# Performance work log

Measured on AMD Instinct MI355X. Metric: run time of the kernel, lower is better.

## Reference

```python
import jax, jax.numpy as jnp
import numpy as np

EMBED_DIM = 1024
NUM_HEADS = 16
HEAD_DIM = EMBED_DIM // NUM_HEADS
SCALE = HEAD_DIM ** 0.5


def setup_inputs() -> dict:
    key = jax.random.key(0)
    kx, kq, kk, kv, ko = jax.random.split(key, 5)
    B, S, D = 4, 2048, EMBED_DIM
    std = 1.0 / np.sqrt(D)
    return {
        "x": jax.random.normal(kx, (B, S, D), dtype=jnp.float32),
        "W_q": jax.random.normal(kq, (D, D), dtype=jnp.float32) * std,
        "W_k": jax.random.normal(kk, (D, D), dtype=jnp.float32) * std,
        "W_v": jax.random.normal(kv, (D, D), dtype=jnp.float32) * std,
        "W_o": jax.random.normal(ko, (D, D), dtype=jnp.float32) * std,
    }


def reference(x, W_q, W_k, W_v, W_o):
    B, S, D = x.shape
    H, Hd = NUM_HEADS, HEAD_DIM

    def split(t):  # [B,S,D] -> [B,H,S,Hd]
        return t.reshape(B, S, H, Hd).transpose(0, 2, 1, 3)

    # nn.Linear stores weight as [out,in] and computes x @ W.T
    Q = split(x @ W_q.T)
    K = split(x @ W_k.T)
    V = split(x @ W_v.T)

    scores = jnp.einsum("bhqd,bhkd->bhqk", Q, K) / SCALE
    causal = jnp.tril(jnp.ones((S, S), dtype=bool))
    scores = jnp.where(causal, scores, -jnp.inf)
    weights = jax.nn.softmax(scores, axis=-1)  # dropout p=0 (eval)
    out = jnp.einsum("bhqk,bhkd->bhqd", weights, V)
    out = out.transpose(0, 2, 1, 3).reshape(B, S, D)
    return out @ W_o.T
```

## Files before the change

### kernel.cpp

```cpp
#include <hip/hip_runtime.h>
#include <stdint.h>

#define DEV __device__ __forceinline__

typedef __bf16 bf16x8 __attribute__((ext_vector_type(8)));
typedef float f32x4 __attribute__((ext_vector_type(4)));

DEV ushort f2bf(float f) {
    union { float f; uint32_t u; } v; v.f = f;
    uint32_t r = v.u + 0x7FFFu + ((v.u >> 16) & 1u);
    return (ushort)(r >> 16);
}

DEV ushort bfc(float f) {
    union { __bf16 h; ushort u; } v;
    v.h = (__bf16)f;
    return v.u;
}

DEV void gld16(const void* g, void* lds) {
    __builtin_amdgcn_global_load_lds(
        (const __attribute__((address_space(1))) void*)g,
        (__attribute__((address_space(3))) void*)lds, 16, 0, 0);
}

DEV bf16x8 ld_frag(const void* p) { return *(const bf16x8*)p; }

__global__ void cvt_kernel(const float* __restrict__ in, ushort* __restrict__ out, int n4) {
    int i = blockIdx.x * blockDim.x + threadIdx.x;
    if (i >= n4) return;
    float4 v = ((const float4*)in)[i];
    ushort4 o;
    o.x = f2bf(v.x); o.y = f2bf(v.y); o.z = f2bf(v.z); o.w = f2bf(v.w);
    ((ushort4*)out)[i] = o;
}

__global__ void cvt4_kernel(const float* __restrict__ w0, const float* __restrict__ w1,
                            const float* __restrict__ w2, const float* __restrict__ w3,
                            ushort* __restrict__ out, int n4) {
    int i = blockIdx.x * blockDim.x + threadIdx.x;
    if (i >= n4) return;
    const float* src = (blockIdx.y == 0) ? w0 : (blockIdx.y == 1) ? w1
                     : (blockIdx.y == 2) ? w2 : w3;
    float4 v = ((const float4*)src)[i];
    ushort4 o;
    o.x = f2bf(v.x); o.y = f2bf(v.y); o.z = f2bf(v.z); o.w = f2bf(v.w);
    ((ushort4*)(out + (size_t)blockIdx.y * n4 * 4))[i] = o;
}

DEV void stage_half(const ushort* Mp, int grow0, int k0, char* ldsbase, int t, int K) {
#pragma unroll
    for (int i = 0; i < 2; ++i) {
        int o = (i * 512 + t) * 16;
        int row = o >> 7;
        int cs = ((o >> 4) & 7) ^ (row & 7);
        gld16((const char*)Mp + ((size_t)(grow0 + row) * K + k0) * 2 + cs * 16, ldsbase + o);
    }
}

DEV void gphase(const char* Ab, const char* Bb, f32x4 acc[8][4],
                int wr, int wc, int rA, int cc, int mh, int nh) {
    bf16x8 af[4][2], bg[2][2];
#pragma unroll
    for (int i2 = 0; i2 < 4; ++i2)
#pragma unroll
        for (int kc = 0; kc < 2; ++kc) {
            int ra = wr * 128 + mh * 64 + i2 * 16 + rA;
            af[i2][kc] = ld_frag(Ab + ra * 128 + (((kc * 4 + cc) ^ (ra & 7)) * 16));
        }
#pragma unroll
    for (int j2 = 0; j2 < 2; ++j2)
#pragma unroll
        for (int kc = 0; kc < 2; ++kc) {
            int rb = wc * 64 + nh * 32 + j2 * 16 + rA;
            bg[j2][kc] = ld_frag(Bb + rb * 128 + (((kc * 4 + cc) ^ (rb & 7)) * 16));
        }
    __builtin_amdgcn_s_setprio(1);
#pragma unroll
    for (int kc = 0; kc < 2; ++kc)
#pragma unroll
        for (int i2 = 0; i2 < 4; ++i2)
#pragma unroll
            for (int j2 = 0; j2 < 2; ++j2)
                acc[mh * 4 + i2][nh * 2 + j2] = __builtin_amdgcn_mfma_f32_16x16x32_bf16(
                    af[i2][kc], bg[j2][kc], acc[mh * 4 + i2][nh * 2 + j2], 0, 0, 0);
    __builtin_amdgcn_s_setprio(0);
}

template<int F32OUT>
__global__ __launch_bounds__(512, 2) void gemm256(const ushort* __restrict__ A,
                                                  const ushort* __restrict__ B,
                                                  void* __restrict__ C,
                                                  int M, int N, int K) {
    __shared__ __align__(16) ushort S[2][2][16384];
    const int G = gridDim.x;
    const int bid = blockIdx.x;
    const int swz = (bid & 7) * (G >> 3) + (bid >> 3);
    const int nbn = N >> 8;
    const int bm = swz / nbn, bn = swz % nbn;
    const int t = threadIdx.x, l = t & 63, w = t >> 6;
    const int wr = w >> 2, wc = w & 3;
    const int rA = l & 15, cc = l >> 4;
    f32x4 acc[8][4] = {};
    const int NT = K >> 6;

    stage_half(A, bm * 256,       0, (char*)S[0][0],         t, K);
    stage_half(A, bm * 256 + 128, 0, (char*)S[0][0] + 16384, t, K);
    stage_half(B, bn * 256,       0, (char*)S[0][1],         t, K);
    stage_half(B, bn * 256 + 128, 0, (char*)S[0][1] + 16384, t, K);
    asm volatile("s_waitcnt vmcnt(0)" ::: "memory");
    __builtin_amdgcn_s_barrier();

    for (int kt = 0; kt < NT; ++kt) {
        const int buf = kt & 1;
        const char* Ab = (const char*)S[buf][0];
        const char* Bb = (const char*)S[buf][1];
        char* An = (char*)S[buf ^ 1][0];
        char* Bn = (char*)S[buf ^ 1][1];
        const int k1 = (kt + 1) << 6;
        const bool more = (kt + 1 < NT);
        if (more) stage_half(A, bm * 256,       k1, An,         t, K);
        gphase(Ab, Bb, acc, wr, wc, rA, cc, 0, 0);
        if (more) stage_half(A, bm * 256 + 128, k1, An + 16384, t, K);
        gphase(Ab, Bb, acc, wr, wc, rA, cc, 0, 1);
        if (more) stage_half(B, bn * 256,       k1, Bn,         t, K);
        gphase(Ab, Bb, acc, wr, wc, rA, cc, 1, 0);
        if (more) stage_half(B, bn * 256 + 128, k1, Bn + 16384, t, K);
        gphase(Ab, Bb, acc, wr, wc, rA, cc, 1, 1);
        asm volatile("s_waitcnt vmcnt(0)" ::: "memory");
        __builtin_amdgcn_s_barrier();
    }

#pragma unroll
    for (int i = 0; i < 8; ++i)
#pragma unroll
        for (int j = 0; j < 4; ++j)
#pragma unroll
            for (int r = 0; r < 4; ++r) {
                int row = bm * 256 + wr * 128 + i * 16 + cc * 4 + r;
                int col = bn * 256 + wc * 64 + j * 16 + rA;
                if (F32OUT) ((float*)C)[(size_t)row * N + col] = acc[i][j][r];
                else        ((ushort*)C)[(size_t)row * N + col] = f2bf(acc[i][j][r]);
            }
}

template<int F32OUT>
__global__ __launch_bounds__(256) void gemm_bt(const ushort* __restrict__ A,
                                               const ushort* __restrict__ B,
                                               void* __restrict__ C,
                                               int M, int N, int K) {
    __shared__ __align__(16) ushort As[128 * 64];
    __shared__ __align__(16) ushort Bs[128 * 64];
    const int G = gridDim.x;
    const int bid = blockIdx.x;
    const int swz = (bid & 7) * (G >> 3) + (bid >> 3);
    const int bm = swz & 63, bn = swz >> 6;
    const int t = threadIdx.x, l = t & 63, w = t >> 6;
    const int wm = w >> 1, wn = w & 1;
    const int rA = l & 15, cc = l >> 4;
    f32x4 acc[4][4] = {};

    for (int k0 = 0; k0 < K; k0 += 64) {
#pragma unroll
        for (int i = 0; i < 4; ++i) {
            int o = (w * 4 + i) * 1024 + l * 16;
            int row = o >> 7, ch = (o >> 4) & 7;
            int cs = ch ^ (row & 7);
            const char* ga = (const char*)A + (((size_t)(bm * 128 + row)) * K + k0) * 2 + cs * 16;
            gld16(ga, (char*)As + (w * 4 + i) * 1024);
            const char* gb = (const char*)B + (((size_t)(bn * 128 + row)) * K + k0) * 2 + cs * 16;
            gld16(gb, (char*)Bs + (w * 4 + i) * 1024);
        }
        __syncthreads();
        bf16x8 af[4][2], bfr[4][2];
#pragma unroll
        for (int i = 0; i < 4; ++i) {
#pragma unroll
            for (int kc = 0; kc < 2; ++kc) {
                int ra = wm * 64 + i * 16 + rA;
                int ca = (kc * 4 + cc) ^ (ra & 7);
                af[i][kc] = ld_frag((const char*)As + ra * 128 + ca * 16);
                int rb = wn * 64 + i * 16 + rA;
                int cb = (kc * 4 + cc) ^ (rb & 7);
                bfr[i][kc] = ld_frag((const char*)Bs + rb * 128 + cb * 16);
            }
        }
#pragma unroll
        for (int kc = 0; kc < 2; ++kc)
#pragma unroll
            for (int i = 0; i < 4; ++i)
#pragma unroll
                for (int j = 0; j < 4; ++j)
                    acc[i][j] = __builtin_amdgcn_mfma_f32_16x16x32_bf16(
                        af[i][kc], bfr[j][kc], acc[i][j], 0, 0, 0);
        __syncthreads();
    }
#pragma unroll
    for (int i = 0; i < 4; ++i)
#pragma unroll
        for (int j = 0; j < 4; ++j)
#pragma unroll
            for (int r = 0; r < 4; ++r) {
                int row = bm * 128 + wm * 64 + i * 16 + cc * 4 + r;
                int col = bn * 128 + wn * 64 + j * 16 + rA;
                if (F32OUT) ((float*)C)[(size_t)row * N + col] = acc[i][j][r];
                else        ((ushort*)C)[(size_t)row * N + col] = f2bf(acc[i][j][r]);
            }
}

__global__ __launch_bounds__(256) void vtrans_kernel(const ushort* __restrict__ qkv,
                                                     ushort* __restrict__ vt) {
    __shared__ ushort tile[64][68];
    const int st = blockIdx.x, bh = blockIdx.y;
    const int b = bh >> 4, h = bh & 15;
    const int t = threadIdx.x;
    const ushort* src = qkv + (size_t)(b * 2048 + st * 64) * 3072 + 2048 + h * 64;
#pragma unroll
    for (int i = 0; i < 2; ++i) {
        int idx = t + i * 256;
        int s = idx >> 3, d0 = (idx & 7) * 8;
        uint4 v = *(const uint4*)(src + (size_t)s * 3072 + d0);
        *(uint2*)&tile[s][d0]     = make_uint2(v.x, v.y);
        *(uint2*)&tile[s][d0 + 4] = make_uint2(v.z, v.w);
    }
    __syncthreads();
    ushort* dst = vt + (size_t)bh * 64 * 2048 + st * 64;
#pragma unroll
    for (int i = 0; i < 2; ++i) {
        int idx = t + i * 256;
        int d = idx >> 3, s0 = (idx & 7) * 8;
        ushort tmp[8];
#pragma unroll
        for (int j = 0; j < 8; ++j) tmp[j] = tile[s0 + j][d];
        *(uint4*)(dst + (size_t)d * 2048 + s0) = *(uint4*)tmp;
    }
}

DEV void stage_kv(const char* Kg0, const char* Vg0, int kv0,
                  char* KsB, char* VsB, int t) {
    int row = t >> 3;
    int cs = (t & 7) ^ (row & 7);
    gld16(Kg0 + (size_t)(kv0 + row) * 6144 + cs * 16, KsB + t * 16);
    gld16(Vg0 + (size_t)row * 4096 + (size_t)kv0 * 2 + cs * 16, VsB + t * 16);
}

DEV void attn_tile(const char* KsB, const char* VsB, char* PsW,
                   const bf16x8* qf, f32x4* oacc, float& lsum,
                   int rA, int cc, int qg, int kv0, bool diag) {
    f32x4 s[4] = {};
    __builtin_amdgcn_s_setprio(1);
#pragma unroll
    for (int kc = 0; kc < 2; ++kc)
#pragma unroll
        for (int c = 0; c < 4; ++c) {
            int rk = c * 16 + rA;
            int ck = (kc * 4 + cc) ^ (rk & 7);
            bf16x8 ak = ld_frag(KsB + rk * 128 + ck * 16);
            s[c] = __builtin_amdgcn_mfma_f32_16x16x32_bf16(ak, qf[kc], s[c], 0, 0, 0);
        }
    __builtin_amdgcn_s_setprio(0);
    const float SC = 0.18033688011116013f;
    const int swz = (rA & 7) << 4;
#pragma unroll
    for (int c = 0; c < 4; ++c) {
        float pv[4];
#pragma unroll
        for (int r = 0; r < 4; ++r) {
            float v = s[c][r] * SC;
            if (diag && (kv0 + c * 16 + cc * 4 + r > qg)) v = -1e30f;
            pv[r] = __builtin_amdgcn_exp2f(v);
            lsum += pv[r];
        }
        union { ushort us[4]; uint2 u2; } pk;
        pk.us[0] = bfc(pv[0]); pk.us[1] = bfc(pv[1]);
        pk.us[2] = bfc(pv[2]); pk.us[3] = bfc(pv[3]);
        *(uint2*)(PsW + rA * 128 + ((32 * c + 8 * cc) ^ swz)) = pk.u2;
    }
    bf16x8 ap[2];
    ap[0] = ld_frag(PsW + rA * 128 + ((16 * cc) ^ swz));
    ap[1] = ld_frag(PsW + rA * 128 + ((64 + 16 * cc) ^ swz));
    __builtin_amdgcn_s_setprio(1);
#pragma unroll
    for (int kc = 0; kc < 2; ++kc)
#pragma unroll
        for (int g = 0; g < 4; ++g) {
            int rv = g * 16 + rA;
            int cv = (kc * 4 + cc) ^ (rv & 7);
            bf16x8 av = ld_frag(VsB + rv * 128 + cv * 16);
            oacc[g] = __builtin_amdgcn_mfma_f32_16x16x32_bf16(av, ap[kc], oacc[g], 0, 0, 0);
        }
    __builtin_amdgcn_s_setprio(0);
}

__global__ __launch_bounds__(512, 4) void attn_kernel(const ushort* __restrict__ qkv,
                                                      const ushort* __restrict__ vt,
                                                      ushort* __restrict__ o_out) {
    const int i = blockIdx.x;
    const int xcd = i & 7, slot = i >> 3;
    const int p = slot >> 3;
    const int bh = ((slot & 7) << 3) | xcd;
    const int ftq = 15 - p;
    const int b = bh >> 4, h = bh & 15;
    const int t = threadIdx.x, l = t & 63, w = t >> 6;
    const int rA = l & 15, cc = l >> 4;
    const int wq16 = w * 16;

    __shared__ __align__(16) ushort Ks[2][64 * 64];
    __shared__ __align__(16) ushort Vs[2][64 * 64];
    __shared__ __align__(16) ushort Ps[8][16 * 64];

    const size_t xbase = (size_t)(b * 2048) * 3072 + (size_t)h * 64;
    const char* Kg0 = (const char*)(qkv + xbase + 1024);
    const char* Vg0 = (const char*)(vt + (size_t)bh * 64 * 2048);

    const int qgN = p * 128 + wq16 + rA;
    const int qgF = ftq * 128 + wq16 + rA;

    bf16x8 qfN[2], qfF[2];
    {
        const ushort* qpN = qkv + xbase + (size_t)qgN * 3072;
        const ushort* qpF = qkv + xbase + (size_t)qgF * 3072;
        qfN[0] = *(const bf16x8*)(qpN + cc * 8);
        qfN[1] = *(const bf16x8*)(qpN + 32 + cc * 8);
        qfF[0] = *(const bf16x8*)(qpF + cc * 8);
        qfF[1] = *(const bf16x8*)(qpF + 32 + cc * 8);
    }
    f32x4 oN[4] = {}, oF[4] = {};
    float lN = 0.f, lF = 0.f;

    const int nkv = 32 - 2 * p;
    stage_kv(Kg0, Vg0, 0, (char*)Ks[0], (char*)Vs[0], t);
    asm volatile("s_waitcnt vmcnt(0)" ::: "memory");
    __builtin_amdgcn_s_barrier();

    for (int kt = 0; kt < nkv; ++kt) {
        const int cur = kt & 1;
        if (kt + 1 < nkv)
            stage_kv(Kg0, Vg0, (kt + 1) * 64, (char*)Ks[cur ^ 1], (char*)Vs[cur ^ 1], t);
        const char* KsB = (const char*)Ks[cur];
        const char* VsB = (const char*)Vs[cur];
        attn_tile(KsB, VsB, (char*)Ps[w], qfF, oF, lF, rA, cc, qgF, kt * 64, kt >= nkv - 2);
        if (kt <= 2 * p + 1)
            attn_tile(KsB, VsB, (char*)Ps[w], qfN, oN, lN, rA, cc, qgN, kt * 64, kt >= 2 * p);
        asm volatile("s_waitcnt vmcnt(0)" ::: "memory");
        __builtin_amdgcn_s_barrier();
    }

    float lf = lF; lf += __shfl_xor(lf, 16); lf += __shfl_xor(lf, 32);
    float ln = lN; ln += __shfl_xor(ln, 16); ln += __shfl_xor(ln, 32);
    const float rf = 1.0f / lf, rn = 1.0f / ln;
    const size_t obF = (size_t)(b * 2048 + qgF) * 1024 + h * 64;
    const size_t obN = (size_t)(b * 2048 + qgN) * 1024 + h * 64;
#pragma unroll
    for (int g = 0; g < 4; ++g) {
        union { ushort us[4]; uint2 u2; } pf, pn;
#pragma unroll
        for (int r = 0; r < 4; ++r) {
            pf.us[r] = bfc(oF[g][r] * rf);
            pn.us[r] = bfc(oN[g][r] * rn);
        }
        *(uint2*)(o_out + obF + 16 * g + 4 * cc) = pf.u2;
        *(uint2*)(o_out + obN + 16 * g + 4 * cc) = pn.u2;
    }
}

extern "C" void kernel_launch(void* const* d_in, const int* in_sizes, int n_in,
                              void* d_out, int out_size, void* d_ws, size_t ws_size,
                              hipStream_t stream) {
    const float* x  = (const float*)d_in[0];
    const float* Wq = (const float*)d_in[1];
    const float* Wk = (const float*)d_in[2];
    const float* Wv = (const float*)d_in[3];
    const float* Wo = (const float*)d_in[4];
    float* out = (float*)d_out;

    const int M = 8192, D = 1024;
    char* ws = (char*)d_ws;
    ushort* xo_bf = (ushort*)ws;
    ushort* wqkv  = (ushort*)(ws + (size_t)M * D * 2);
    ushort* wo_bf = (ushort*)(ws + (size_t)M * D * 2 + (size_t)3 * D * D * 2);
    ushort* qkv   = (ushort*)(ws + (size_t)M * D * 2 + (size_t)4 * D * D * 2);
    ushort* vt    = (ushort*)d_out;

    cvt_kernel<<<dim3(M * D / 4 / 256), 256, 0, stream>>>(x, xo_bf, M * D / 4);
    cvt4_kernel<<<dim3(D * D / 4 / 256, 4), 256, 0, stream>>>(Wq, Wk, Wv, Wo, wqkv, D * D / 4);

    gemm256<0><<<dim3((M / 256) * (3072 / 256)), 512, 0, stream>>>(xo_bf, wqkv, qkv, M, 3072, D);

    vtrans_kernel<<<dim3(32, 64), 256, 0, stream>>>(qkv, vt);

    attn_kernel<<<dim3(512), 512, 0, stream>>>(qkv, vt, xo_bf);

    gemm_bt<1><<<dim3((M / 128) * (D / 128)), 256, 0, stream>>>(xo_bf, wo_bf, out, M, D, D);
}
```

Measured before the change: 244.7 us.

## Fold softmax scale into W_q, compute row sums via MFMA, double-buffer out-proj GEMM

The softmax scale (1/sqrt(d)·log2e) is folded into W_q during bf16 conversion, which removes a per-element multiply in the attention tile. The per-row softmax denominator is now accumulated by an MFMA against a vector of ones instead of scalar adds and cross-lane shuffles. It uses the same bf16-rounded probabilities as the PV product. The 128x128 GEMM gains LDS double-buffering with prefetch of the next K tile and priority hints around its MFMAs. The 256x256 GEMM issues all next-tile loads before compute instead of interleaving them.

```diff
diff --git a/kernel.cpp b/kernel.cpp
--- a/kernel.cpp
+++ b/kernel.cpp
@@ -42,9 +42,11 @@
     if (i >= n4) return;
     const float* src = (blockIdx.y == 0) ? w0 : (blockIdx.y == 1) ? w1
                      : (blockIdx.y == 2) ? w2 : w3;
+    const float scl = (blockIdx.y == 0) ? 0.18033688011116013f : 1.0f;
     float4 v = ((const float4*)src)[i];
     ushort4 o;
-    o.x = f2bf(v.x); o.y = f2bf(v.y); o.z = f2bf(v.z); o.w = f2bf(v.w);
+    o.x = f2bf(v.x * scl); o.y = f2bf(v.y * scl);
+    o.z = f2bf(v.z * scl); o.w = f2bf(v.w * scl);
     ((ushort4*)(out + (size_t)blockIdx.y * n4 * 4))[i] = o;
 }
 
@@ -118,14 +120,15 @@
         char* An = (char*)S[buf ^ 1][0];
         char* Bn = (char*)S[buf ^ 1][1];
         const int k1 = (kt + 1) << 6;
-        const bool more = (kt + 1 < NT);
-        if (more) stage_half(A, bm * 256,       k1, An,         t, K);
+        if (kt + 1 < NT) {
+            stage_half(A, bm * 256,       k1, An,         t, K);
+            stage_half(A, bm * 256 + 128, k1, An + 16384, t, K);
+            stage_half(B, bn * 256,       k1, Bn,         t, K);
+            stage_half(B, bn * 256 + 128, k1, Bn + 16384, t, K);
+        }
         gphase(Ab, Bb, acc, wr, wc, rA, cc, 0, 0);
-        if (more) stage_half(A, bm * 256 + 128, k1, An + 16384, t, K);
         gphase(Ab, Bb, acc, wr, wc, rA, cc, 0, 1);
-        if (more) stage_half(B, bn * 256,       k1, Bn,         t, K);
         gphase(Ab, Bb, acc, wr, wc, rA, cc, 1, 0);
-        if (more) stage_half(B, bn * 256 + 128, k1, Bn + 16384, t, K);
         gphase(Ab, Bb, acc, wr, wc, rA, cc, 1, 1);
         asm volatile("s_waitcnt vmcnt(0)" ::: "memory");
         __builtin_amdgcn_s_barrier();
@@ -149,8 +152,8 @@
                                                const ushort* __restrict__ B,
                                                void* __restrict__ C,
                                                int M, int N, int K) {
-    __shared__ __align__(16) ushort As[128 * 64];
-    __shared__ __align__(16) ushort Bs[128 * 64];
+    __shared__ __align__(16) ushort As[2][128 * 64];
+    __shared__ __align__(16) ushort Bs[2][128 * 64];
     const int G = gridDim.x;
     const int bid = blockIdx.x;
     const int swz = (bid & 7) * (G >> 3) + (bid >> 3);
@@ -159,32 +162,43 @@
     const int wm = w >> 1, wn = w & 1;
     const int rA = l & 15, cc = l >> 4;
     f32x4 acc[4][4] = {};
-
-    for (int k0 = 0; k0 < K; k0 += 64) {
-#pragma unroll
-        for (int i = 0; i < 4; ++i) {
-            int o = (w * 4 + i) * 1024 + l * 16;
-            int row = o >> 7, ch = (o >> 4) & 7;
-            int cs = ch ^ (row & 7);
-            const char* ga = (const char*)A + (((size_t)(bm * 128 + row)) * K + k0) * 2 + cs * 16;
-            gld16(ga, (char*)As + (w * 4 + i) * 1024);
-            const char* gb = (const char*)B + (((size_t)(bn * 128 + row)) * K + k0) * 2 + cs * 16;
-            gld16(gb, (char*)Bs + (w * 4 + i) * 1024);
-        }
-        __syncthreads();
+    const int NT = K >> 6;
+
+#define STAGE_AB(k0, sb)                                                              \
+    {                                                                                  \
+        _Pragma("unroll")                                                              \
+        for (int i = 0; i < 4; ++i) {                                                  \
+            int o = (w * 4 + i) * 1024 + l * 16;                                       \
+            int row = o >> 7;                                                          \
+            int cs = ((o >> 4) & 7) ^ (row & 7);                                       \
+            gld16((const char*)A + (((size_t)(bm * 128 + row)) * K + (k0)) * 2 + cs * 16, \
+                  (char*)As[sb] + o);                                                  \
+            gld16((const char*)B + (((size_t)(bn * 128 + row)) * K + (k0)) * 2 + cs * 16, \
+                  (char*)Bs[sb] + o);                                                  \
+        }                                                                              \
+    }
+
+    STAGE_AB(0, 0);
+    asm volatile("s_waitcnt vmcnt(0)" ::: "memory");
+    __builtin_amdgcn_s_barrier();
+
+    for (int kt = 0; kt < NT; ++kt) {
+        const int sb = kt & 1;
+        if (kt + 1 < NT) STAGE_AB((kt + 1) << 6, sb ^ 1);
+        const char* Ab = (const char*)As[sb];
+        const char* Bb = (const char*)Bs[sb];
         bf16x8 af[4][2], bfr[4][2];
 #pragma unroll
         for (int i = 0; i < 4; ++i) {
 #pragma unroll
             for (int kc = 0; kc < 2; ++kc) {
                 int ra = wm * 64 + i * 16 + rA;
-                int ca = (kc * 4 + cc) ^ (ra & 7);
-                af[i][kc] = ld_frag((const char*)As + ra * 128 + ca * 16);
+                af[i][kc] = ld_frag(Ab + ra * 128 + (((kc * 4 + cc) ^ (ra & 7)) * 16));
                 int rb = wn * 64 + i * 16 + rA;
-                int cb = (kc * 4 + cc) ^ (rb & 7);
-                bfr[i][kc] = ld_frag((const char*)Bs + rb * 128 + cb * 16);
+                bfr[i][kc] = ld_frag(Bb + rb * 128 + (((kc * 4 + cc) ^ (rb & 7)) * 16));
             }
         }
+        __builtin_amdgcn_s_setprio(1);
 #pragma unroll
         for (int kc = 0; kc < 2; ++kc)
 #pragma unroll
@@ -193,8 +207,11 @@
                 for (int j = 0; j < 4; ++j)
                     acc[i][j] = __builtin_amdgcn_mfma_f32_16x16x32_bf16(
                         af[i][kc], bfr[j][kc], acc[i][j], 0, 0, 0);
-        __syncthreads();
-    }
+        __builtin_amdgcn_s_setprio(0);
+        asm volatile("s_waitcnt vmcnt(0)" ::: "memory");
+        __builtin_amdgcn_s_barrier();
+    }
+#undef STAGE_AB
 #pragma unroll
     for (int i = 0; i < 4; ++i)
 #pragma unroll
@@ -245,7 +262,7 @@
 }
 
 DEV void attn_tile(const char* KsB, const char* VsB, char* PsW,
-                   const bf16x8* qf, f32x4* oacc, float& lsum,
+                   const bf16x8* qf, f32x4* oacc, f32x4& osum, const bf16x8 ones,
                    int rA, int cc, int qg, int kv0, bool diag) {
     f32x4 s[4] = {};
     __builtin_amdgcn_s_setprio(1);
@@ -259,17 +276,15 @@
             s[c] = __builtin_amdgcn_mfma_f32_16x16x32_bf16(ak, qf[kc], s[c], 0, 0, 0);
         }
     __builtin_amdgcn_s_setprio(0);
-    const float SC = 0.18033688011116013f;
     const int swz = (rA & 7) << 4;
 #pragma unroll
     for (int c = 0; c < 4; ++c) {
         float pv[4];
 #pragma unroll
         for (int r = 0; r < 4; ++r) {
-            float v = s[c][r] * SC;
+            float v = s[c][r];
             if (diag && (kv0 + c * 16 + cc * 4 + r > qg)) v = -1e30f;
             pv[r] = __builtin_amdgcn_exp2f(v);
-            lsum += pv[r];
         }
         union { ushort us[4]; uint2 u2; } pk;
         pk.us[0] = bfc(pv[0]); pk.us[1] = bfc(pv[1]);
@@ -280,6 +295,8 @@
     ap[0] = ld_frag(PsW + rA * 128 + ((16 * cc) ^ swz));
     ap[1] = ld_frag(PsW + rA * 128 + ((64 + 16 * cc) ^ swz));
     __builtin_amdgcn_s_setprio(1);
+    osum = __builtin_amdgcn_mfma_f32_16x16x32_bf16(ones, ap[0], osum, 0, 0, 0);
+    osum = __builtin_amdgcn_mfma_f32_16x16x32_bf16(ones, ap[1], osum, 0, 0, 0);
 #pragma unroll
     for (int kc = 0; kc < 2; ++kc)
 #pragma unroll
@@ -325,8 +342,12 @@
         qfF[0] = *(const bf16x8*)(qpF + cc * 8);
         qfF[1] = *(const bf16x8*)(qpF + 32 + cc * 8);
     }
+    bf16x8 ones;
+#pragma unroll
+    for (int z = 0; z < 8; ++z) ones[z] = (__bf16)1.0f;
+
     f32x4 oN[4] = {}, oF[4] = {};
-    float lN = 0.f, lF = 0.f;
+    f32x4 osN = {}, osF = {};
 
     const int nkv = 32 - 2 * p;
     stage_kv(Kg0, Vg0, 0, (char*)Ks[0], (char*)Vs[0], t);
@@ -339,16 +360,14 @@
             stage_kv(Kg0, Vg0, (kt + 1) * 64, (char*)Ks[cur ^ 1], (char*)Vs[cur ^ 1], t);
         const char* KsB = (const char*)Ks[cur];
         const char* VsB = (const char*)Vs[cur];
-        attn_tile(KsB, VsB, (char*)Ps[w], qfF, oF, lF, rA, cc, qgF, kt * 64, kt >= nkv - 2);
+        attn_tile(KsB, VsB, (char*)Ps[w], qfF, oF, osF, ones, rA, cc, qgF, kt * 64, kt >= nkv - 2);
         if (kt <= 2 * p + 1)
-            attn_tile(KsB, VsB, (char*)Ps[w], qfN, oN, lN, rA, cc, qgN, kt * 64, kt >= 2 * p);
+            attn_tile(KsB, VsB, (char*)Ps[w], qfN, oN, osN, ones, rA, cc, qgN, kt * 64, kt >= 2 * p);
         asm volatile("s_waitcnt vmcnt(0)" ::: "memory");
         __builtin_amdgcn_s_barrier();
     }
 
-    float lf = lF; lf += __shfl_xor(lf, 16); lf += __shfl_xor(lf, 32);
-    float ln = lN; ln += __shfl_xor(ln, 16); ln += __shfl_xor(ln, 32);
-    const float rf = 1.0f / lf, rn = 1.0f / ln;
+    const float rf = 1.0f / osF[0], rn = 1.0f / osN[0];
     const size_t obF = (size_t)(b * 2048 + qgF) * 1024 + h * 64;
     const size_t obN = (size_t)(b * 2048 + qgN) * 1024 + h * 64;
 #pragma unroll
```

Result: slower. 251.6 us (+2.8%).
